# Optimization experiments

Hardware: AMD Instinct MI355X
Metric: run time of the kernel (lower is better)

Reference implementation:

```python
import jax, jax.numpy as jnp
import numpy as np

HIDDEN = 1024
NUM_CLASSES = 10
NUM_GAUSSIANS = 8
IN_FEATURES = 16
HEADS = NUM_CLASSES * NUM_GAUSSIANS * IN_FEATURES * 2  # 2560 tiny Linear(hidden,1) heads


def setup_inputs() -> dict:
    key = jax.random.key(0)
    kx, kw, kb = jax.random.split(key, 3)
    x = jax.random.normal(kx, (8192, HIDDEN), dtype=jnp.float32)
    # Stacked weights of the 2560 per-head Linear(hidden,1) layers.
    bound = 1.0 / np.sqrt(HIDDEN)
    W = jax.random.uniform(kw, (HIDDEN, HEADS), minval=-bound, maxval=bound, dtype=jnp.float32)
    b = jax.random.uniform(kb, (HEADS,), minval=-bound, maxval=bound, dtype=jnp.float32)
    return {"x": x, "W": W, "b": b}


def reference(x, W, b):
    batch = x.shape[0]
    # Fused form of the Python loop of Linear(hidden,1)+Sigmoid per head.
    z = jax.nn.sigmoid(x @ W + b)  # [batch, HEADS]
    return z.reshape(batch, NUM_CLASSES, NUM_GAUSSIANS, IN_FEATURES, 2)
```

## Files before the change

### kernel.cpp

```cpp
#include <hip/hip_runtime.h>
#include <hip/hip_bf16.h>

#define HIDDEN 1024
#define HEADS  2560

#define BM 128
#define BN 160
#define BK 64
#define NT (HIDDEN / BK)
#define ABYT (BM * BK * 2)
#define BBYT (BN * BK * 2)
#define BUFSZ (ABYT + BBYT)

typedef float  f32x4  __attribute__((ext_vector_type(4)));
typedef __bf16 bf16x8 __attribute__((ext_vector_type(8)));
typedef __bf16 bf16x4 __attribute__((ext_vector_type(4)));

__device__ __forceinline__ void gload_lds16(const void* g, void* l) {
    __builtin_amdgcn_global_load_lds(
        (const __attribute__((address_space(1))) unsigned int*)g,
        (__attribute__((address_space(3))) unsigned int*)l, 16, 0, 0);
}
__device__ __forceinline__ unsigned swz(unsigned x) {
    return x ^ (((x >> 7) & 7u) << 4);
}

__global__ __launch_bounds__(256)
void cvt_all(const float* __restrict__ x, const float* __restrict__ W,
             __bf16* __restrict__ xc, __bf16* __restrict__ Wt, int n8)
{
    if (blockIdx.x < 640) {
        __shared__ __bf16 tile[64][72];
        const int t  = threadIdx.x;
        const int n0 = (blockIdx.x % 40) * 64;
        const int k0 = (blockIdx.x / 40) * 64;

        #pragma unroll
        for (int i = 0; i < 4; ++i) {
            const int k    = (t >> 4) + i * 16;
            const int col4 = (t & 15) * 4;
            const float4 v = *reinterpret_cast<const float4*>(
                W + (size_t)(k0 + k) * HEADS + n0 + col4);
            bf16x4 h;
            h[0] = (__bf16)v.x; h[1] = (__bf16)v.y; h[2] = (__bf16)v.z; h[3] = (__bf16)v.w;
            *reinterpret_cast<bf16x4*>(&tile[k][col4]) = h;
        }
        __syncthreads();
        #pragma unroll
        for (int i = 0; i < 4; ++i) {
            const int n  = (t >> 4) + i * 16;
            const int k4 = (t & 15) * 4;
            bf16x4 h;
            h[0] = tile[k4 + 0][n]; h[1] = tile[k4 + 1][n];
            h[2] = tile[k4 + 2][n]; h[3] = tile[k4 + 3][n];
            *reinterpret_cast<bf16x4*>(Wt + (size_t)(n0 + n) * HIDDEN + k0 + k4) = h;
        }
    } else {
        int idx    = (blockIdx.x - 640) * blockDim.x + threadIdx.x;
        int stride = (gridDim.x - 640) * blockDim.x;
        for (int i = idx; i < n8; i += stride) {
            const float4 a = *reinterpret_cast<const float4*>(x + (size_t)i * 8);
            const float4 b = *reinterpret_cast<const float4*>(x + (size_t)i * 8 + 4);
            bf16x8 h;
            h[0] = (__bf16)a.x; h[1] = (__bf16)a.y; h[2] = (__bf16)a.z; h[3] = (__bf16)a.w;
            h[4] = (__bf16)b.x; h[5] = (__bf16)b.y; h[6] = (__bf16)b.z; h[7] = (__bf16)b.w;
            *reinterpret_cast<bf16x8*>(xc + (size_t)i * 8) = h;
        }
    }
}

__global__ __launch_bounds__(512, 4)
void gemm_dl2(const __bf16* __restrict__ A, const __bf16* __restrict__ Bt,
              const float* __restrict__ bias, float* __restrict__ out)
{
    __shared__ char lds[2 * BUFSZ];

    const int t    = threadIdx.x;
    const int lane = t & 63;
    const int w    = t >> 6;
    const int wr   = w & 3;
    const int wc   = w >> 2;
    const int lhi  = lane >> 4;
    const int llo  = lane & 15;

    const int bid = blockIdx.x;
    const int by  = (bid & 7) * 2 + ((bid >> 3) & 1);
    const int bx  = bid >> 4;
    const int bm0 = bx * BM;
    const int bn0 = by * BN;

    const unsigned d0 = (unsigned)(t * 16);
    const unsigned L0 = swz(d0);
    const char* asrc0 = (const char*)A  + (size_t)(bm0 + (L0 >> 7)) * (HIDDEN * 2) + (L0 & 127);
    const char* bsrc0 = (const char*)Bt + (size_t)(bn0 + (L0 >> 7)) * (HIDDEN * 2) + (L0 & 127);
    const unsigned dt = 16384u + (unsigned)(t * 16);
    const unsigned Lt = swz(dt);
    const char* bsrct = (const char*)Bt + (size_t)(bn0 + (Lt >> 7)) * (HIDDEN * 2) + (Lt & 127);

    char* adst0 = (char*)lds + d0;
    char* bdst0 = (char*)lds + ABYT + d0;
    char* bdstt = (char*)lds + ABYT + dt;

    const unsigned xa = (unsigned)((llo & 7) << 4);
    const unsigned klo[2] = { ((unsigned)(lhi * 16)) ^ xa,
                              ((unsigned)(64 + lhi * 16)) ^ xa };
    const unsigned rowA = (unsigned)((wr * 32 + llo) * 128);
    const unsigned rowB = (unsigned)ABYT + (unsigned)((wc * 80 + llo) * 128);

    f32x4 acc[2][5];
    #pragma unroll
    for (int m = 0; m < 2; ++m)
        #pragma unroll
        for (int n = 0; n < 5; ++n)
            acc[m][n] = f32x4{0.f, 0.f, 0.f, 0.f};

    gload_lds16(asrc0,          adst0);
    gload_lds16(asrc0 + 131072, adst0 + 8192);
    gload_lds16(bsrc0,          bdst0);
    gload_lds16(bsrc0 + 131072, bdst0 + 8192);
    if (w < 4) gload_lds16(bsrct, bdstt);
    asm volatile("s_waitcnt vmcnt(0)" ::: "memory");
    __builtin_amdgcn_s_barrier();

    for (int k = 0; k < NT; ++k) {
        const char* buf  = lds + (k & 1) * BUFSZ;
        const unsigned nb = (unsigned)(((k + 1) & 1) * BUFSZ);
        const int   koff = (k + 1) * 128;

        if (k + 1 < NT) {
            gload_lds16(asrc0 + koff,          adst0 + nb);
            gload_lds16(asrc0 + koff + 131072, adst0 + nb + 8192);
            gload_lds16(bsrc0 + koff,          bdst0 + nb);
            gload_lds16(bsrc0 + koff + 131072, bdst0 + nb + 8192);
            if (w < 4) gload_lds16(bsrct + koff, bdstt + nb);
        }

        #pragma unroll
        for (int kk = 0; kk < 2; ++kk) {
            bf16x8 af[2], bfr[5];
            #pragma unroll
            for (int m = 0; m < 2; ++m)
                af[m]  = *(const bf16x8*)(buf + rowA + m * 2048 + klo[kk]);
            #pragma unroll
            for (int n = 0; n < 5; ++n)
                bfr[n] = *(const bf16x8*)(buf + rowB + n * 2048 + klo[kk]);
            #pragma unroll
            for (int m = 0; m < 2; ++m)
                #pragma unroll
                for (int n = 0; n < 5; ++n)
                    acc[m][n] = __builtin_amdgcn_mfma_f32_16x16x32_bf16(
                        af[m], bfr[n], acc[m][n], 0, 0, 0);
        }

        asm volatile("s_waitcnt vmcnt(0)" ::: "memory");
        __builtin_amdgcn_s_barrier();
    }

    #pragma unroll
    for (int n = 0; n < 5; ++n) {
        const int col  = bn0 + wc * 80 + n * 16 + llo;
        const float bv = bias[col];
        #pragma unroll
        for (int m = 0; m < 2; ++m) {
            const int row0 = bm0 + wr * 32 + m * 16 + lhi * 4;
            #pragma unroll
            for (int r = 0; r < 4; ++r) {
                const float z = acc[m][n][r] + bv;
                out[(size_t)(row0 + r) * HEADS + col] = __fdividef(1.0f, 1.0f + __expf(-z));
            }
        }
    }
}

#define FBM 128
#define FBN 128
#define FBK 32
#define FLDK 40

__global__ __launch_bounds__(256)
void lch_gemm(const float* __restrict__ x, const float* __restrict__ W,
              const float* __restrict__ b, float* __restrict__ out)
{
    __shared__ __bf16 As[FBM][FLDK];
    __shared__ __bf16 Bs[FBN][FLDK];

    const int t   = threadIdx.x;
    const int bm0 = blockIdx.x * FBM;
    const int bn0 = blockIdx.y * FBN;
    const int lane = t & 63;
    const int wid  = t >> 6;
    const int wr   = wid >> 1;
    const int wc   = wid & 1;
    const int lhi  = lane >> 4;
    const int llo  = lane & 15;

    f32x4 acc[4][4];
    #pragma unroll
    for (int i = 0; i < 4; ++i)
        #pragma unroll
        for (int j = 0; j < 4; ++j)
            acc[i][j] = f32x4{0.f, 0.f, 0.f, 0.f};

    const int bn_col  = t & 127;
    const int bk_base = (t >> 7) * 16;

    for (int k0 = 0; k0 < HIDDEN; k0 += FBK) {
        #pragma unroll
        for (int i = 0; i < 4; ++i) {
            const int f   = t + i * 256;
            const int row = f >> 3;
            const int c4  = (f & 7) * 4;
            const float4 v = *reinterpret_cast<const float4*>(
                x + (size_t)(bm0 + row) * HIDDEN + k0 + c4);
            bf16x4 h;
            h[0] = (__bf16)v.x; h[1] = (__bf16)v.y;
            h[2] = (__bf16)v.z; h[3] = (__bf16)v.w;
            *reinterpret_cast<bf16x4*>(&As[row][c4]) = h;
        }
        {
            const float* wp = W + (size_t)(k0 + bk_base) * HEADS + bn0 + bn_col;
            bf16x8 h0, h1;
            #pragma unroll
            for (int i = 0; i < 8; ++i) h0[i] = (__bf16)wp[(size_t)i * HEADS];
            #pragma unroll
            for (int i = 0; i < 8; ++i) h1[i] = (__bf16)wp[(size_t)(i + 8) * HEADS];
            *reinterpret_cast<bf16x8*>(&Bs[bn_col][bk_base])     = h0;
            *reinterpret_cast<bf16x8*>(&Bs[bn_col][bk_base + 8]) = h1;
        }
        __syncthreads();

        bf16x8 af[4], bfr[4];
        #pragma unroll
        for (int i = 0; i < 4; ++i)
            af[i] = *reinterpret_cast<const bf16x8*>(&As[wr * 64 + i * 16 + llo][lhi * 8]);
        #pragma unroll
        for (int j = 0; j < 4; ++j)
            bfr[j] = *reinterpret_cast<const bf16x8*>(&Bs[wc * 64 + j * 16 + llo][lhi * 8]);
        #pragma unroll
        for (int i = 0; i < 4; ++i)
            #pragma unroll
            for (int j = 0; j < 4; ++j)
                acc[i][j] = __builtin_amdgcn_mfma_f32_16x16x32_bf16(
                    af[i], bfr[j], acc[i][j], 0, 0, 0);
        __syncthreads();
    }

    #pragma unroll
    for (int j = 0; j < 4; ++j) {
        const int col  = bn0 + wc * 64 + j * 16 + llo;
        const float bv = b[col];
        #pragma unroll
        for (int i = 0; i < 4; ++i) {
            const int row0 = bm0 + wr * 64 + i * 16 + lhi * 4;
            #pragma unroll
            for (int r = 0; r < 4; ++r) {
                const float z = acc[i][j][r] + bv;
                out[(size_t)(row0 + r) * HEADS + col] = 1.0f / (1.0f + __expf(-z));
            }
        }
    }
}

extern "C" void kernel_launch(void* const* d_in, const int* in_sizes, int n_in,
                              void* d_out, int out_size, void* d_ws, size_t ws_size,
                              hipStream_t stream) {
    const float* x = (const float*)d_in[0];
    const float* W = (const float*)d_in[1];
    const float* b = (const float*)d_in[2];
    float* out     = (float*)d_out;

    const int M = in_sizes[0] / HIDDEN;

    const size_t xc_bytes = (size_t)M * HIDDEN * sizeof(__bf16);
    const size_t wt_bytes = (size_t)HEADS * HIDDEN * sizeof(__bf16);

    if (ws_size >= xc_bytes + wt_bytes && (M % BM) == 0) {
        __bf16* xc = (__bf16*)d_ws;
        __bf16* Wt = (__bf16*)((char*)d_ws + xc_bytes);

        cvt_all<<<640 + 2048, 256, 0, stream>>>(x, W, xc, Wt, M * HIDDEN / 8);

        const int nwg = (M / BM) * (HEADS / BN);
        gemm_dl2<<<nwg, 512, 0, stream>>>(xc, Wt, b, out);
    } else {
        dim3 grid(M / FBM, HEADS / FBN);
        lch_gemm<<<grid, dim3(256), 0, stream>>>(x, W, b, out);
    }
}
```

Baseline: 66.83 us.

## Enlarge GEMM macro-tile to 256x320 with 2x4 wave layout and MFMA priority

Quadruples the workgroup output tile from 128x160 to 256x320. Each of the 8 waves now computes a 128x80 slab (8x5 MFMA tiles) instead of 32x80, which raises arithmetic intensity per LDS fragment load and halves global re-reads of A and B. It also brackets the MFMA loop with s_setprio. The costs are a 4x larger accumulator register footprint (160 VGPRs of accumulators), larger LDS use (double-buffered 72KB), occupancy reduced to 2 workgroups per CU, and only 256 workgroups total for 256 CUs, which risks tail and latency exposure.

```diff
diff --git a/kernel.cpp b/kernel.cpp
--- a/kernel.cpp
+++ b/kernel.cpp
@@ -4,8 +4,8 @@
 #define HIDDEN 1024
 #define HEADS  2560
 
-#define BM 128
-#define BN 160
+#define BM 256
+#define BN 320
 #define BK 64
 #define NT (HIDDEN / BK)
 #define ABYT (BM * BK * 2)
@@ -69,8 +69,8 @@
     }
 }
 
-__global__ __launch_bounds__(512, 4)
-void gemm_dl2(const __bf16* __restrict__ A, const __bf16* __restrict__ Bt,
+__global__ __launch_bounds__(512, 2)
+void gemm_big(const __bf16* __restrict__ A, const __bf16* __restrict__ Bt,
               const float* __restrict__ bias, float* __restrict__ out)
 {
     __shared__ char lds[2 * BUFSZ];
@@ -78,14 +78,14 @@
     const int t    = threadIdx.x;
     const int lane = t & 63;
     const int w    = t >> 6;
-    const int wr   = w & 3;
-    const int wc   = w >> 2;
+    const int wr   = w >> 2;
+    const int wc   = w & 3;
     const int lhi  = lane >> 4;
     const int llo  = lane & 15;
 
     const int bid = blockIdx.x;
-    const int by  = (bid & 7) * 2 + ((bid >> 3) & 1);
-    const int bx  = bid >> 4;
+    const int by  = bid & 7;
+    const int bx  = bid >> 3;
     const int bm0 = bx * BM;
     const int bn0 = by * BN;
 
@@ -93,32 +93,26 @@
     const unsigned L0 = swz(d0);
     const char* asrc0 = (const char*)A  + (size_t)(bm0 + (L0 >> 7)) * (HIDDEN * 2) + (L0 & 127);
     const char* bsrc0 = (const char*)Bt + (size_t)(bn0 + (L0 >> 7)) * (HIDDEN * 2) + (L0 & 127);
-    const unsigned dt = 16384u + (unsigned)(t * 16);
-    const unsigned Lt = swz(dt);
-    const char* bsrct = (const char*)Bt + (size_t)(bn0 + (Lt >> 7)) * (HIDDEN * 2) + (Lt & 127);
-
     char* adst0 = (char*)lds + d0;
     char* bdst0 = (char*)lds + ABYT + d0;
-    char* bdstt = (char*)lds + ABYT + dt;
 
     const unsigned xa = (unsigned)((llo & 7) << 4);
     const unsigned klo[2] = { ((unsigned)(lhi * 16)) ^ xa,
                               ((unsigned)(64 + lhi * 16)) ^ xa };
-    const unsigned rowA = (unsigned)((wr * 32 + llo) * 128);
-    const unsigned rowB = (unsigned)ABYT + (unsigned)((wc * 80 + llo) * 128);
-
-    f32x4 acc[2][5];
-    #pragma unroll
-    for (int m = 0; m < 2; ++m)
+    const unsigned rowA = (unsigned)(wr * 16384 + llo * 128);
+    const unsigned rowB = (unsigned)ABYT + (unsigned)(wc * 10240 + llo * 128);
+
+    f32x4 acc[8][5];
+    #pragma unroll
+    for (int m = 0; m < 8; ++m)
         #pragma unroll
         for (int n = 0; n < 5; ++n)
             acc[m][n] = f32x4{0.f, 0.f, 0.f, 0.f};
 
-    gload_lds16(asrc0,          adst0);
-    gload_lds16(asrc0 + 131072, adst0 + 8192);
-    gload_lds16(bsrc0,          bdst0);
-    gload_lds16(bsrc0 + 131072, bdst0 + 8192);
-    if (w < 4) gload_lds16(bsrct, bdstt);
+    #pragma unroll
+    for (int li = 0; li < 4; ++li) gload_lds16(asrc0 + li * 131072, adst0 + li * 8192);
+    #pragma unroll
+    for (int li = 0; li < 5; ++li) gload_lds16(bsrc0 + li * 131072, bdst0 + li * 8192);
     asm volatile("s_waitcnt vmcnt(0)" ::: "memory");
     __builtin_amdgcn_s_barrier();
 
@@ -128,28 +122,31 @@
         const int   koff = (k + 1) * 128;
 
         if (k + 1 < NT) {
-            gload_lds16(asrc0 + koff,          adst0 + nb);
-            gload_lds16(asrc0 + koff + 131072, adst0 + nb + 8192);
-            gload_lds16(bsrc0 + koff,          bdst0 + nb);
-            gload_lds16(bsrc0 + koff + 131072, bdst0 + nb + 8192);
-            if (w < 4) gload_lds16(bsrct + koff, bdstt + nb);
+            #pragma unroll
+            for (int li = 0; li < 4; ++li)
+                gload_lds16(asrc0 + koff + li * 131072, adst0 + nb + li * 8192);
+            #pragma unroll
+            for (int li = 0; li < 5; ++li)
+                gload_lds16(bsrc0 + koff + li * 131072, bdst0 + nb + li * 8192);
         }
 
         #pragma unroll
         for (int kk = 0; kk < 2; ++kk) {
-            bf16x8 af[2], bfr[5];
-            #pragma unroll
-            for (int m = 0; m < 2; ++m)
+            bf16x8 af[8], bfr[5];
+            #pragma unroll
+            for (int m = 0; m < 8; ++m)
                 af[m]  = *(const bf16x8*)(buf + rowA + m * 2048 + klo[kk]);
             #pragma unroll
             for (int n = 0; n < 5; ++n)
                 bfr[n] = *(const bf16x8*)(buf + rowB + n * 2048 + klo[kk]);
-            #pragma unroll
-            for (int m = 0; m < 2; ++m)
+            __builtin_amdgcn_s_setprio(1);
+            #pragma unroll
+            for (int m = 0; m < 8; ++m)
                 #pragma unroll
                 for (int n = 0; n < 5; ++n)
                     acc[m][n] = __builtin_amdgcn_mfma_f32_16x16x32_bf16(
                         af[m], bfr[n], acc[m][n], 0, 0, 0);
+            __builtin_amdgcn_s_setprio(0);
         }
 
         asm volatile("s_waitcnt vmcnt(0)" ::: "memory");
@@ -161,8 +158,8 @@
         const int col  = bn0 + wc * 80 + n * 16 + llo;
         const float bv = bias[col];
         #pragma unroll
-        for (int m = 0; m < 2; ++m) {
-            const int row0 = bm0 + wr * 32 + m * 16 + lhi * 4;
+        for (int m = 0; m < 8; ++m) {
+            const int row0 = bm0 + wr * 128 + m * 16 + lhi * 4;
             #pragma unroll
             for (int r = 0; r < 4; ++r) {
                 const float z = acc[m][n][r] + bv;
@@ -281,7 +278,7 @@
         cvt_all<<<640 + 2048, 256, 0, stream>>>(x, W, xc, Wt, M * HIDDEN / 8);
 
         const int nwg = (M / BM) * (HEADS / BN);
-        gemm_dl2<<<nwg, 512, 0, stream>>>(xc, Wt, b, out);
+        gemm_big<<<nwg, 512, 0, stream>>>(xc, Wt, b, out);
     } else {
         dim3 grid(M / FBM, HEADS / FBN);
         lch_gemm<<<grid, dim3(256), 0, stream>>>(x, W, b, out);
```

Result: faster. 65.30 us (-2.3%).

## Load A fragments directly into registers, keep only B in LDS

Applied to the files above, without the earlier changes.

The A operand tile no longer goes through LDS. Each lane prefetches its MFMA A fragments straight from global memory into registers one K-step ahead, and LDS now holds only a double-buffered B tile. The block-to-tile mapping is reordered into groups of eight M-tiles, and the MFMA burst is wrapped in s_setprio. This cuts LDS footprint and LDS read traffic, at the cost of extra VGPRs and duplicated global/L2 reads of A across the two column-waves.

```diff
diff --git a/kernel.cpp b/kernel.cpp
--- a/kernel.cpp
+++ b/kernel.cpp
@@ -8,9 +8,7 @@
 #define BN 160
 #define BK 64
 #define NT (HIDDEN / BK)
-#define ABYT (BM * BK * 2)
 #define BBYT (BN * BK * 2)
-#define BUFSZ (ABYT + BBYT)
 
 typedef float  f32x4  __attribute__((ext_vector_type(4)));
 typedef __bf16 bf16x8 __attribute__((ext_vector_type(8)));
@@ -70,10 +68,10 @@
 }
 
 __global__ __launch_bounds__(512, 4)
-void gemm_dl2(const __bf16* __restrict__ A, const __bf16* __restrict__ Bt,
-              const float* __restrict__ bias, float* __restrict__ out)
+void gemm_ar(const __bf16* __restrict__ A, const __bf16* __restrict__ Bt,
+             const float* __restrict__ bias, float* __restrict__ out)
 {
-    __shared__ char lds[2 * BUFSZ];
+    __shared__ char lds[2 * BBYT];
 
     const int t    = threadIdx.x;
     const int lane = t & 63;
@@ -84,28 +82,28 @@
     const int llo  = lane & 15;
 
     const int bid = blockIdx.x;
-    const int by  = (bid & 7) * 2 + ((bid >> 3) & 1);
-    const int bx  = bid >> 4;
+    const int q   = bid >> 3;
+    const int bx  = (bid & 7) * 8 + (q & 7);
+    const int by  = q >> 3;
     const int bm0 = bx * BM;
     const int bn0 = by * BN;
 
     const unsigned d0 = (unsigned)(t * 16);
     const unsigned L0 = swz(d0);
-    const char* asrc0 = (const char*)A  + (size_t)(bm0 + (L0 >> 7)) * (HIDDEN * 2) + (L0 & 127);
     const char* bsrc0 = (const char*)Bt + (size_t)(bn0 + (L0 >> 7)) * (HIDDEN * 2) + (L0 & 127);
     const unsigned dt = 16384u + (unsigned)(t * 16);
     const unsigned Lt = swz(dt);
     const char* bsrct = (const char*)Bt + (size_t)(bn0 + (Lt >> 7)) * (HIDDEN * 2) + (Lt & 127);
-
-    char* adst0 = (char*)lds + d0;
-    char* bdst0 = (char*)lds + ABYT + d0;
-    char* bdstt = (char*)lds + ABYT + dt;
+    char* bdst0 = (char*)lds + d0;
+    char* bdstt = (char*)lds + dt;
+
+    const char* a_lane = (const char*)A
+        + (size_t)(bm0 + wr * 32 + llo) * (HIDDEN * 2) + lhi * 16;
 
     const unsigned xa = (unsigned)((llo & 7) << 4);
     const unsigned klo[2] = { ((unsigned)(lhi * 16)) ^ xa,
                               ((unsigned)(64 + lhi * 16)) ^ xa };
-    const unsigned rowA = (unsigned)((wr * 32 + llo) * 128);
-    const unsigned rowB = (unsigned)ABYT + (unsigned)((wc * 80 + llo) * 128);
+    const unsigned rowB = (unsigned)(wc * 10240 + llo * 128);
 
     f32x4 acc[2][5];
     #pragma unroll
@@ -114,42 +112,55 @@
         for (int n = 0; n < 5; ++n)
             acc[m][n] = f32x4{0.f, 0.f, 0.f, 0.f};
 
-    gload_lds16(asrc0,          adst0);
-    gload_lds16(asrc0 + 131072, adst0 + 8192);
+    bf16x8 afn[2][2], afc[2][2];
+
     gload_lds16(bsrc0,          bdst0);
     gload_lds16(bsrc0 + 131072, bdst0 + 8192);
     if (w < 4) gload_lds16(bsrct, bdstt);
+    #pragma unroll
+    for (int m = 0; m < 2; ++m)
+        #pragma unroll
+        for (int kk = 0; kk < 2; ++kk)
+            afn[m][kk] = *(const bf16x8*)(a_lane + m * 32768 + kk * 64);
     asm volatile("s_waitcnt vmcnt(0)" ::: "memory");
     __builtin_amdgcn_s_barrier();
 
     for (int k = 0; k < NT; ++k) {
-        const char* buf  = lds + (k & 1) * BUFSZ;
-        const unsigned nb = (unsigned)(((k + 1) & 1) * BUFSZ);
+        const char* buf  = lds + (k & 1) * BBYT;
+        const unsigned nb = (unsigned)(((k + 1) & 1) * BBYT);
         const int   koff = (k + 1) * 128;
 
+        #pragma unroll
+        for (int m = 0; m < 2; ++m)
+            #pragma unroll
+            for (int kk = 0; kk < 2; ++kk)
+                afc[m][kk] = afn[m][kk];
+
         if (k + 1 < NT) {
-            gload_lds16(asrc0 + koff,          adst0 + nb);
-            gload_lds16(asrc0 + koff + 131072, adst0 + nb + 8192);
             gload_lds16(bsrc0 + koff,          bdst0 + nb);
             gload_lds16(bsrc0 + koff + 131072, bdst0 + nb + 8192);
             if (w < 4) gload_lds16(bsrct + koff, bdstt + nb);
+            #pragma unroll
+            for (int m = 0; m < 2; ++m)
+                #pragma unroll
+                for (int kk = 0; kk < 2; ++kk)
+                    afn[m][kk] = *(const bf16x8*)(a_lane + m * 32768 + kk * 64 + koff);
         }
 
         #pragma unroll
         for (int kk = 0; kk < 2; ++kk) {
-            bf16x8 af[2], bfr[5];
-            #pragma unroll
-            for (int m = 0; m < 2; ++m)
-                af[m]  = *(const bf16x8*)(buf + rowA + m * 2048 + klo[kk]);
+            bf16x8 bfr[5];
             #pragma unroll
             for (int n = 0; n < 5; ++n)
                 bfr[n] = *(const bf16x8*)(buf + rowB + n * 2048 + klo[kk]);
+            __builtin_amdgcn_s_setprio(1);
             #pragma unroll
             for (int m = 0; m < 2; ++m)
                 #pragma unroll
                 for (int n = 0; n < 5; ++n)
                     acc[m][n] = __builtin_amdgcn_mfma_f32_16x16x32_bf16(
-                        af[m], bfr[n], acc[m][n], 0, 0, 0);
+                        afc[m][kk], bfr[n], acc[m][n], 0, 0, 0);
+            __builtin_amdgcn_s_setprio(0);
         }
 
         asm volatile("s_waitcnt vmcnt(0)" ::: "memory");
@@ -281,7 +292,7 @@
         cvt_all<<<640 + 2048, 256, 0, stream>>>(x, W, xc, Wt, M * HIDDEN / 8);
 
         const int nwg = (M / BM) * (HEADS / BN);
-        gemm_dl2<<<nwg, 512, 0, stream>>>(xc, Wt, b, out);
+        gemm_ar<<<nwg, 512, 0, stream>>>(xc, Wt, b, out);
     } else {
         dim3 grid(M / FBM, HEADS / FBN);
         lch_gemm<<<grid, dim3(256), 0, stream>>>(x, W, b, out);
```

After: 97.12 us. 45.3% more time.

## Retile bf16 GEMM to 256x128x32 blocks with 4x4 MFMA per wave

Applied to the files above, without the earlier changes.

The bf16 MFMA GEMM moves from 128x160x64 tiles to 256x128x32 tiles. Each wave now computes a 64x64 sub-tile with 4x4 accumulators instead of 32x80, and the LDS swizzle and load mapping are adjusted for 64-byte rows. The block-to-tile mapping is also changed to an XCD-strided order (blockIdx & 7, times 80). The aim is more arithmetic per LDS fragment load and a simpler load pattern, at the cost of smaller K steps, which means more barriers per tile, plus more accumulator registers.

```diff
diff --git a/kernel.cpp b/kernel.cpp
--- a/kernel.cpp
+++ b/kernel.cpp
@@ -4,9 +4,9 @@
 #define HIDDEN 1024
 #define HEADS  2560
 
-#define BM 128
-#define BN 160
-#define BK 64
+#define BM 256
+#define BN 128
+#define BK 32
 #define NT (HIDDEN / BK)
 #define ABYT (BM * BK * 2)
 #define BBYT (BN * BK * 2)
@@ -22,7 +22,7 @@
         (__attribute__((address_space(3))) unsigned int*)l, 16, 0, 0);
 }
 __device__ __forceinline__ unsigned swz(unsigned x) {
-    return x ^ (((x >> 7) & 7u) << 4);
+    return x ^ (((x >> 6) & 3u) << 4);
 }
 
 __global__ __launch_bounds__(256)
@@ -70,8 +70,8 @@
 }
 
 __global__ __launch_bounds__(512, 4)
-void gemm_dl2(const __bf16* __restrict__ A, const __bf16* __restrict__ Bt,
-              const float* __restrict__ bias, float* __restrict__ out)
+void gemm_sq(const __bf16* __restrict__ A, const __bf16* __restrict__ Bt,
+             const float* __restrict__ bias, float* __restrict__ out)
 {
     __shared__ char lds[2 * BUFSZ];
 
@@ -83,86 +83,73 @@
     const int lhi  = lane >> 4;
     const int llo  = lane & 15;
 
-    const int bid = blockIdx.x;
-    const int by  = (bid & 7) * 2 + ((bid >> 3) & 1);
-    const int bx  = bid >> 4;
+    const int g   = (blockIdx.x & 7) * 80 + (blockIdx.x >> 3);
+    const int bx  = g / 20;
+    const int by  = g % 20;
     const int bm0 = bx * BM;
     const int bn0 = by * BN;
 
     const unsigned d0 = (unsigned)(t * 16);
-    const unsigned L0 = swz(d0);
-    const char* asrc0 = (const char*)A  + (size_t)(bm0 + (L0 >> 7)) * (HIDDEN * 2) + (L0 & 127);
-    const char* bsrc0 = (const char*)Bt + (size_t)(bn0 + (L0 >> 7)) * (HIDDEN * 2) + (L0 & 127);
-    const unsigned dt = 16384u + (unsigned)(t * 16);
-    const unsigned Lt = swz(dt);
-    const char* bsrct = (const char*)Bt + (size_t)(bn0 + (Lt >> 7)) * (HIDDEN * 2) + (Lt & 127);
-
+    const unsigned r0 = d0 >> 6;
+    const unsigned c0 = (d0 & 63) ^ ((r0 & 3u) << 4);
+    const char* asrc0 = (const char*)A  + (size_t)(bm0 + r0) * (HIDDEN * 2) + c0;
+    const char* bsrc0 = (const char*)Bt + (size_t)(bn0 + r0) * (HIDDEN * 2) + c0;
     char* adst0 = (char*)lds + d0;
     char* bdst0 = (char*)lds + ABYT + d0;
-    char* bdstt = (char*)lds + ABYT + dt;
-
-    const unsigned xa = (unsigned)((llo & 7) << 4);
-    const unsigned klo[2] = { ((unsigned)(lhi * 16)) ^ xa,
-                              ((unsigned)(64 + lhi * 16)) ^ xa };
-    const unsigned rowA = (unsigned)((wr * 32 + llo) * 128);
-    const unsigned rowB = (unsigned)ABYT + (unsigned)((wc * 80 + llo) * 128);
-
-    f32x4 acc[2][5];
-    #pragma unroll
-    for (int m = 0; m < 2; ++m)
-        #pragma unroll
-        for (int n = 0; n < 5; ++n)
+
+    const unsigned klo  = ((unsigned)(lhi * 16)) ^ ((unsigned)((llo & 3) << 4));
+    const unsigned rowA = (unsigned)((wr * 64 + llo) * 64);
+    const unsigned rowB = (unsigned)ABYT + (unsigned)((wc * 64 + llo) * 64);
+
+    f32x4 acc[4][4];
+    #pragma unroll
+    for (int m = 0; m < 4; ++m)
+        #pragma unroll
+        for (int n = 0; n < 4; ++n)
             acc[m][n] = f32x4{0.f, 0.f, 0.f, 0.f};
 
     gload_lds16(asrc0,          adst0);
-    gload_lds16(asrc0 + 131072, adst0 + 8192);
+    gload_lds16(asrc0 + 262144, adst0 + 8192);
     gload_lds16(bsrc0,          bdst0);
-    gload_lds16(bsrc0 + 131072, bdst0 + 8192);
-    if (w < 4) gload_lds16(bsrct, bdstt);
     asm volatile("s_waitcnt vmcnt(0)" ::: "memory");
     __builtin_amdgcn_s_barrier();
 
     for (int k = 0; k < NT; ++k) {
         const char* buf  = lds + (k & 1) * BUFSZ;
         const unsigned nb = (unsigned)(((k + 1) & 1) * BUFSZ);
-        const int   koff = (k + 1) * 128;
+        const int   koff = (k + 1) * 64;
 
         if (k + 1 < NT) {
             gload_lds16(asrc0 + koff,          adst0 + nb);
-            gload_lds16(asrc0 + koff + 131072, adst0 + nb + 8192);
+            gload_lds16(asrc0 + koff + 262144, adst0 + nb + 8192);
             gload_lds16(bsrc0 + koff,          bdst0 + nb);
-            gload_lds16(bsrc0 + koff + 131072, bdst0 + nb + 8192);
-            if (w < 4) gload_lds16(bsrct + koff, bdstt + nb);
-        }
-
-        #pragma unroll
-        for (int kk = 0; kk < 2; ++kk) {
-            bf16x8 af[2], bfr[5];
-            #pragma unroll
-            for (int m = 0; m < 2; ++m)
-                af[m]  = *(const bf16x8*)(buf + rowA + m * 2048 + klo[kk]);
-            #pragma unroll
-            for (int n = 0; n < 5; ++n)
-                bfr[n] = *(const bf16x8*)(buf + rowB + n * 2048 + klo[kk]);
-            #pragma unroll
-            for (int m = 0; m < 2; ++m)
-                #pragma unroll
-                for (int n = 0; n < 5; ++n)
-                    acc[m][n] = __builtin_amdgcn_mfma_f32_16x16x32_bf16(
-                        af[m], bfr[n], acc[m][n], 0, 0, 0);
-        }
+        }
+
+        bf16x8 af[4], bfr[4];
+        #pragma unroll
+        for (int m = 0; m < 4; ++m)
+            af[m]  = *(const bf16x8*)(buf + rowA + m * 1024 + klo);
+        #pragma unroll
+        for (int n = 0; n < 4; ++n)
+            bfr[n] = *(const bf16x8*)(buf + rowB + n * 1024 + klo);
+        #pragma unroll
+        for (int m = 0; m < 4; ++m)
+            #pragma unroll
+            for (int n = 0; n < 4; ++n)
+                acc[m][n] = __builtin_amdgcn_mfma_f32_16x16x32_bf16(
+                    af[m], bfr[n], acc[m][n], 0, 0, 0);
 
         asm volatile("s_waitcnt vmcnt(0)" ::: "memory");
         __builtin_amdgcn_s_barrier();
     }
 
     #pragma unroll
-    for (int n = 0; n < 5; ++n) {
-        const int col  = bn0 + wc * 80 + n * 16 + llo;
+    for (int n = 0; n < 4; ++n) {
+        const int col  = bn0 + wc * 64 + n * 16 + llo;
         const float bv = bias[col];
         #pragma unroll
-        for (int m = 0; m < 2; ++m) {
-            const int row0 = bm0 + wr * 32 + m * 16 + lhi * 4;
+        for (int m = 0; m < 4; ++m) {
+            const int row0 = bm0 + wr * 64 + m * 16 + lhi * 4;
             #pragma unroll
             for (int r = 0; r < 4; ++r) {
                 const float z = acc[m][n][r] + bv;
@@ -281,7 +268,7 @@
         cvt_all<<<640 + 2048, 256, 0, stream>>>(x, W, xc, Wt, M * HIDDEN / 8);
 
         const int nwg = (M / BM) * (HEADS / BN);
-        gemm_dl2<<<nwg, 512, 0, stream>>>(xc, Wt, b, out);
+        gemm_sq<<<nwg, 512, 0, stream>>>(xc, Wt, b, out);
     } else {
         dim3 grid(M / FBM, HEADS / FBN);
         lch_gemm<<<grid, dim3(256), 0, stream>>>(x, W, b, out);
```

Result: slower. 81.20 us (+21.5%).
